# Performance work log

Measured on AMD Instinct MI355X. Metric: run time of the kernel, lower is better.

The kernel has to match this reference:

```python
import jax, jax.numpy as jnp
import numpy as np

B, MAX_S, HID = 128, 4096, 5120
H, D_NOPE, D_ROPE, D_V = 128, 128, 64, 128
KV_SIZE = 512 + 64  # kv_lora_rank + qk_rope_head_dim = 576


def setup_inputs() -> dict:
    key = jax.random.key(0)
    ks = jax.random.split(key, 8)
    seq_lens = jax.random.randint(ks[0], (B,), 1, MAX_S)
    return {
        "hidden_states": jax.random.normal(ks[1], (B, 1, HID), jnp.float32),
        "k_cache": jax.random.normal(ks[2], (B, MAX_S, D_NOPE), jnp.float32),
        "v_cache": jax.random.normal(ks[3], (B, MAX_S, D_V), jnp.float32),
        "Wq": jax.random.normal(ks[4], (HID, H * (D_NOPE + D_ROPE)), jnp.float32) * 0.02,
        "Wkv": jax.random.normal(ks[5], (HID, KV_SIZE), jnp.float32) * 0.02,
        "Wo": jax.random.normal(ks[6], (H * D_V, HID), jnp.float32) * 0.02,
        "positions": seq_lens - 1,
        "slot_mapping": seq_lens - 1,
        "seq_lens": seq_lens,
    }


def reference(hidden_states, k_cache, v_cache, Wq, Wkv, Wo, positions, slot_mapping, seq_lens):
    h = hidden_states[:, -1, :]                        # [B, HID] last-token decode
    q = (h @ Wq).reshape(B, H, D_NOPE + D_ROPE)        # [B, H, 192]
    kv = h @ Wkv                                       # [B, 576]
    q_nope = q[:, :, :D_NOPE]                          # [B, H, 128]
    k_new = kv[:, :D_NOPE]                             # [B, 128]
    v_new = kv[:, D_NOPE:D_NOPE + D_V]                 # [B, 128]

    b_idx = jnp.arange(B)
    kc = k_cache.at[b_idx, slot_mapping].set(k_new)    # write new token into paged cache
    vc = v_cache.at[b_idx, slot_mapping].set(v_new)

    scale = D_NOPE ** -0.5
    scores = jnp.einsum('bhd,bsd->bhs', q_nope, kc) * scale  # MQA: 1 kv head broadcast
    valid = jnp.arange(MAX_S)[None, :] < seq_lens[:, None]   # [B, S]
    scores = jnp.where(valid[:, None, :], scores, jnp.float32(-1e30))
    p = jax.nn.softmax(scores, axis=-1)
    attn = jnp.einsum('bhs,bsd->bhd', p, vc)           # [B, H, 128]

    return attn.reshape(B, 1, H * D_V) @ Wo            # [B, 1, HID]
```

## Files before the change

### kernel.cpp

```cpp
#include <hip/hip_runtime.h>
#include <hip/hip_bf16.h>

typedef __attribute__((ext_vector_type(4))) float f32x4;
typedef __attribute__((ext_vector_type(8))) short bf16x8;
typedef __attribute__((ext_vector_type(2))) unsigned int u32x2;
typedef __attribute__((ext_vector_type(4))) unsigned int u32x4;

static __device__ __forceinline__ unsigned short f2bf(float f) {
    unsigned u = __builtin_bit_cast(unsigned, f);
    u += 0x7fffu + ((u >> 16) & 1u);
    return (unsigned short)(u >> 16);
}
static __device__ __forceinline__ unsigned pack2(float a, float b) {
    __hip_bfloat162 h = __float22bfloat162_rn(make_float2(a, b));
    unsigned u;
    __builtin_memcpy(&u, &h, 4);
    return u;
}

static __device__ __forceinline__ void bar_nodrain() {
    __builtin_amdgcn_sched_barrier(0);
    asm volatile("s_waitcnt lgkmcnt(0)" ::: "memory");
    __builtin_amdgcn_s_barrier();
    __builtin_amdgcn_sched_barrier(0);
}

__global__ __launch_bounds__(256)
void cvt_bf16(const float* __restrict__ in, unsigned* __restrict__ out, int n8)
{
    const int i = blockIdx.x * 256 + threadIdx.x;
    if (i >= n8) return;
    f32x4 a = ((const f32x4*)in)[2 * i];
    f32x4 b = ((const f32x4*)in)[2 * i + 1];
    u32x4 p = { pack2(a[0], a[1]), pack2(a[2], a[3]), pack2(b[0], b[1]), pack2(b[2], b[3]) };
    ((u32x4*)out)[i] = p;
}

template<int COLMAP>
__global__ __launch_bounds__(256, 4)
void gemm128(const unsigned short* __restrict__ Ah, int lda,
             const float* __restrict__ Bm, int ldb,
             float* __restrict__ Cp, int ldc,
             int kchunk, int nsplit)
{
    __shared__ __align__(16) unsigned short As[128 * 72];
    __shared__ __align__(16) unsigned short Bs[64 * 66];

    const int tid = threadIdx.x;
    const int w = tid >> 6, l = tid & 63, lg = l >> 4, l15 = l & 15;
    const int bx = blockIdx.x / nsplit;
    const int by = blockIdx.x % nsplit;
    const int n0 = bx * 64;
    const int pcol = COLMAP ? ((n0 >> 7) * 192 + (n0 & 127)) : n0;
    const size_t k0base = (size_t)by * (size_t)kchunk;
    float* __restrict__ C = Cp + (size_t)by * ((size_t)128 * (size_t)ldc);

    const int ar = tid >> 1;
    const int ac = (tid & 1) * 32;
    const int bnb = (tid & 15) * 4;
    const int bkk = tid >> 4;

    u32x4 aReg[4];
    f32x4 b0Reg[2][2], b1Reg[2][2];

    auto loadA = [&](size_t k0) {
#pragma unroll
        for (int k = 0; k < 4; k++)
            aReg[k] = *(const u32x4*)(Ah + (size_t)ar * lda + k0 + ac + 8 * k);
    };
    auto storeA = [&]() {
#pragma unroll
        for (int k = 0; k < 4; k++)
            *(u32x4*)&As[ar * 72 + ac + 8 * k] = aReg[k];
    };
    auto loadB = [&](f32x4 (&bR)[2][2], size_t k0) {
#pragma unroll
        for (int i = 0; i < 2; i++) {
            const float* bp = Bm + (k0 + (size_t)(2 * (bkk + 16 * i))) * (size_t)ldb + pcol + bnb;
            bR[i][0] = *(const f32x4*)bp;
            bR[i][1] = *(const f32x4*)(bp + ldb);
        }
    };
    auto storeB = [&](f32x4 (&bR)[2][2]) {
        unsigned* bd = (unsigned*)Bs;
#pragma unroll
        for (int i = 0; i < 2; i++)
#pragma unroll
            for (int j = 0; j < 4; j++)
                bd[(bnb + j) * 33 + bkk + 16 * i] = pack2(bR[i][0][j], bR[i][1][j]);
    };

    f32x4 acc[2][4];
    const f32x4 fzero = {0.f, 0.f, 0.f, 0.f};
#pragma unroll
    for (int a = 0; a < 2; a++)
#pragma unroll
        for (int b2 = 0; b2 < 4; b2++) acc[a][b2] = fzero;

    auto mfmaStep = [&]() {
#pragma unroll
        for (int ks = 0; ks < 2; ks++) {
            bf16x8 bfr[4];
#pragma unroll
            for (int nf = 0; nf < 4; nf++)
                bfr[nf] = *(const bf16x8*)&Bs[(16 * nf + l15) * 66 + 32 * ks + 8 * lg];
#pragma unroll
            for (int mf = 0; mf < 2; mf++) {
                bf16x8 af = *(const bf16x8*)&As[(32 * w + 16 * mf + l15) * 72 + 32 * ks + 8 * lg];
#pragma unroll
                for (int nf = 0; nf < 4; nf++)
                    acc[mf][nf] = __builtin_amdgcn_mfma_f32_16x16x32_bf16(af, bfr[nf], acc[mf][nf], 0, 0, 0);
            }
        }
    };

    const int nst = kchunk >> 6;
    auto kof = [&](int t) { return k0base + (size_t)(t << 6); };

    loadA(kof(0));
    loadB(b0Reg, kof(0));
    if (nst > 1) loadB(b1Reg, kof(1));

    for (int t = 0; t < nst; t += 2) {
        storeA(); storeB(b0Reg);
        bar_nodrain();
        if (t + 1 < nst) loadA(kof(t + 1));
        if (t + 2 < nst) loadB(b0Reg, kof(t + 2));
        __builtin_amdgcn_sched_barrier(0);
        mfmaStep();
        bar_nodrain();
        if (t + 1 < nst) {
            storeA(); storeB(b1Reg);
            bar_nodrain();
            if (t + 2 < nst) loadA(kof(t + 2));
            if (t + 3 < nst) loadB(b1Reg, kof(t + 3));
            __builtin_amdgcn_sched_barrier(0);
            mfmaStep();
            bar_nodrain();
        }
    }
#pragma unroll
    for (int mf = 0; mf < 2; mf++) {
#pragma unroll
        for (int nf = 0; nf < 4; nf++) {
            const int m0 = 32 * w + 16 * mf + 4 * lg;
            const int cn = n0 + 16 * nf + l15;
#pragma unroll
            for (int r = 0; r < 4; r++)
                C[(size_t)(m0 + r) * ldc + cn] = acc[mf][nf][r];
        }
    }
}

__global__ __launch_bounds__(256)
void reduce_f32(const float* __restrict__ in, float* __restrict__ out, int n4, int ns)
{
    const int i = blockIdx.x * 256 + threadIdx.x;
    if (i >= n4) return;
    const f32x4* in4 = (const f32x4*)in;
    f32x4 s = in4[i];
    for (int j = 1; j < ns; j++) s += in4[i + (size_t)j * n4];
    ((f32x4*)out)[i] = s;
}

__global__ __launch_bounds__(256)
void reduce_q_bf16(const float* __restrict__ in, unsigned* __restrict__ out)
{
    const int i = blockIdx.x * 256 + threadIdx.x;
    const f32x4* in4 = (const f32x4*)in;
    f32x4 s = in4[i] + in4[i + 524288] + in4[i + 2 * 524288] + in4[i + 3 * 524288];
    const float scale = 0.088388347648318447f;
    s *= scale;
    u32x2 p = { pack2(s[0], s[1]), pack2(s[2], s[3]) };
    *(u32x2*)&out[2 * i] = p;
}

#define NSPLIT 8
#define CHUNK_T 8
#define KVSPLIT 16

__global__ __launch_bounds__(512, 4)
void attn_fwd(const float* __restrict__ kc, const float* __restrict__ vc,
              const unsigned short* __restrict__ qb, const float* __restrict__ kvp,
              const int* __restrict__ seq_lens, const int* __restrict__ slot_map,
              float* __restrict__ Opart, float* __restrict__ m_ws, float* __restrict__ l_ws)
{
    __shared__ __align__(16) unsigned short Ks [64 * 136];
    __shared__ __align__(16) unsigned short Vts[128 * 72];
    __shared__ __align__(16) unsigned short Ps [128 * 72];
    __shared__ float knew_s[128];
    __shared__ float vnew_s[128];

    const int b = blockIdx.x, split = blockIdx.y;
    const int seq = seq_lens[b], slot = slot_map[b];
    const int nt = (seq + 63) >> 6;
    const int t0 = split * CHUNK_T;
    const int t1 = min(t0 + CHUNK_T, nt);
    const int slotTile = slot >> 6;

    const int tid = threadIdx.x, w = tid >> 6, l = tid & 63, lg = l >> 4, l15 = l & 15;
    const int h = 16 * w + l15;

    float m_run = -__builtin_inff(), l_run = 0.0f;

    if (t0 < t1) {
        if (slotTile >= t0 && slotTile < t1 && tid < 256) {
            float s = 0.f;
#pragma unroll
            for (int j = 0; j < KVSPLIT; j++) s += kvp[j * 32768 + b * 256 + tid];
            if (tid < 128) knew_s[tid] = s;
            else           vnew_s[tid - 128] = s;
        }

        bf16x8 qf[4];
        {
            const unsigned short* qrow = qb + (size_t)b * 16384 + (size_t)h * 128;
#pragma unroll
            for (int ks = 0; ks < 4; ks++)
                qf[ks] = *(const bf16x8*)(qrow + 32 * ks + 8 * lg);
        }

        f32x4 kReg[4];
        f32x4 vReg[2][2];
        const int kr  = tid >> 3;
        const int kcb = (tid & 7) * 16;
        const int vsp = tid & 31;
        const int vdq = tid >> 5;

        auto loadKV = [&](int t) {
            const int s0 = t << 6;
            const float* ksrc = kc + ((size_t)b * 4096 + s0 + kr) * 128 + kcb;
#pragma unroll
            for (int c = 0; c < 4; c++) kReg[c] = *(const f32x4*)(ksrc + 4 * c);
#pragma unroll
            for (int i = 0; i < 2; i++) {
                const int d4 = 4 * vdq + 64 * i;
                const float* r1 = vc + ((size_t)b * 4096 + s0 + 2 * vsp) * 128 + d4;
                vReg[i][0] = *(const f32x4*)r1;
                vReg[i][1] = *(const f32x4*)(r1 + 128);
            }
        };
        auto storeKV = [&]() {
            u32x4 w0 = { pack2(kReg[0][0], kReg[0][1]), pack2(kReg[0][2], kReg[0][3]),
                         pack2(kReg[1][0], kReg[1][1]), pack2(kReg[1][2], kReg[1][3]) };
            u32x4 w1 = { pack2(kReg[2][0], kReg[2][1]), pack2(kReg[2][2], kReg[2][3]),
                         pack2(kReg[3][0], kReg[3][1]), pack2(kReg[3][2], kReg[3][3]) };
            *(u32x4*)&Ks[kr * 136 + kcb] = w0;
            *(u32x4*)&Ks[kr * 136 + kcb + 8] = w1;
            unsigned* vt = (unsigned*)Vts;
#pragma unroll
            for (int i = 0; i < 2; i++)
#pragma unroll
                for (int j = 0; j < 4; j++)
                    vt[(4 * vdq + 64 * i + j) * 36 + vsp] = pack2(vReg[i][0][j], vReg[i][1][j]);
        };

        f32x4 accO[8];
        const f32x4 fzero = {0.f, 0.f, 0.f, 0.f};
#pragma unroll
        for (int i = 0; i < 8; i++) accO[i] = fzero;

        loadKV(t0);
        for (int t = t0; t < t1; ++t) {
            const int s0 = t << 6;
            storeKV();
            bar_nodrain();
            if (t == slotTile) {
                if (tid < 128) {
                    const int sloc = slot & 63;
                    Ks [sloc * 136 + tid] = f2bf(knew_s[tid]);
                    Vts[tid * 72 + sloc]  = f2bf(vnew_s[tid]);
                }
                bar_nodrain();
            }
            if (t + 1 < t1) loadKV(t + 1);
            __builtin_amdgcn_sched_barrier(0);

            f32x4 accS[4];
#pragma unroll
            for (int sf = 0; sf < 4; sf++) accS[sf] = fzero;
#pragma unroll
            for (int ks = 0; ks < 4; ks++) {
#pragma unroll
                for (int sf = 0; sf < 4; sf++) {
                    bf16x8 kf = *(const bf16x8*)&Ks[(16 * sf + l15) * 136 + 32 * ks + 8 * lg];
                    accS[sf] = __builtin_amdgcn_mfma_f32_16x16x32_bf16(kf, qf[ks], accS[sf], 0, 0, 0);
                }
            }
            float tmax = -__builtin_inff();
#pragma unroll
            for (int sf = 0; sf < 4; sf++) {
#pragma unroll
                for (int r = 0; r < 4; r++) {
                    const int s = s0 + 16 * sf + 4 * lg + r;
                    float sc = (s < seq) ? accS[sf][r] : -__builtin_inff();
                    accS[sf][r] = sc;
                    tmax = fmaxf(tmax, sc);
                }
            }
            tmax = fmaxf(tmax, __shfl_xor(tmax, 16));
            tmax = fmaxf(tmax, __shfl_xor(tmax, 32));
            const float mnew = fmaxf(m_run, tmax);
            const float so = __expf(m_run - mnew);
            float lsum = 0.f;
#pragma unroll
            for (int sf = 0; sf < 4; sf++) {
#pragma unroll
                for (int r = 0; r < 4; r++) {
                    const float p = __expf(accS[sf][r] - mnew);
                    accS[sf][r] = p;
                    lsum += p;
                }
            }
            lsum += __shfl_xor(lsum, 16);
            lsum += __shfl_xor(lsum, 32);
            l_run = l_run * so + lsum;
            m_run = mnew;
#pragma unroll
            for (int i = 0; i < 8; i++) accO[i] *= so;

            {
                unsigned* pd = (unsigned*)Ps;
#pragma unroll
                for (int sf = 0; sf < 4; sf++) {
                    pd[h * 36 + 8 * sf + 2 * lg + 0] = pack2(accS[sf][0], accS[sf][1]);
                    pd[h * 36 + 8 * sf + 2 * lg + 1] = pack2(accS[sf][2], accS[sf][3]);
                }
            }
            bf16x8 pf[2];
#pragma unroll
            for (int ks = 0; ks < 2; ks++)
                pf[ks] = *(const bf16x8*)&Ps[h * 72 + 32 * ks + 8 * lg];
#pragma unroll
            for (int df = 0; df < 8; df++) {
#pragma unroll
                for (int ks = 0; ks < 2; ks++) {
                    bf16x8 vf = *(const bf16x8*)&Vts[(16 * df + l15) * 72 + 32 * ks + 8 * lg];
                    accO[df] = __builtin_amdgcn_mfma_f32_16x16x32_bf16(vf, pf[ks], accO[df], 0, 0, 0);
                }
            }
            bar_nodrain();
        }
        const size_t base = ((size_t)(b * NSPLIT + split)) * 16384 + (size_t)h * 128;
#pragma unroll
        for (int df = 0; df < 8; df++)
            *(f32x4*)&Opart[base + 16 * df + 4 * lg] = accO[df];
    }
    if (lg == 0) {
        m_ws[(b * NSPLIT + split) * 128 + h] = m_run;
        l_ws[(b * NSPLIT + split) * 128 + h] = l_run;
    }
}

__global__ __launch_bounds__(256)
void combine8(const float* __restrict__ Opart, const float* __restrict__ m_ws,
              const float* __restrict__ l_ws, unsigned* __restrict__ attn_bf)
{
    const int idx = blockIdx.x * 256 + threadIdx.x;
    const int d4 = (idx & 31) * 4;
    const int hh = (idx >> 5) & 127;
    const int b = idx >> 12;

    float m = -__builtin_inff();
    float mv[NSPLIT], lv[NSPLIT];
#pragma unroll
    for (int j = 0; j < NSPLIT; j++) {
        mv[j] = m_ws[(b * NSPLIT + j) * 128 + hh];
        lv[j] = l_ws[(b * NSPLIT + j) * 128 + hh];
        m = fmaxf(m, mv[j]);
    }
    f32x4 o = {0.f, 0.f, 0.f, 0.f};
    float lsum = 0.f;
#pragma unroll
    for (int j = 0; j < NSPLIT; j++) {
        const float a = (lv[j] > 0.f) ? __expf(mv[j] - m) : 0.f;
        lsum += a * lv[j];
        if (a > 0.f) {
            f32x4 oj = *(const f32x4*)&Opart[((size_t)(b * NSPLIT + j)) * 16384 + (size_t)hh * 128 + d4];
            o += oj * a;
        }
    }
    o *= (1.0f / lsum);
    u32x2 p = { pack2(o[0], o[1]), pack2(o[2], o[3]) };
    *(u32x2*)&attn_bf[(size_t)b * 8192 + (size_t)hh * 64 + (d4 >> 1)] = p;
}

extern "C" void kernel_launch(void* const* d_in, const int* in_sizes, int n_in,
                              void* d_out, int out_size, void* d_ws, size_t ws_size,
                              hipStream_t stream)
{
    const float* hidden  = (const float*)d_in[0];
    const float* k_cache = (const float*)d_in[1];
    const float* v_cache = (const float*)d_in[2];
    const float* Wq      = (const float*)d_in[3];
    const float* Wkv     = (const float*)d_in[4];
    const float* Wo      = (const float*)d_in[5];
    const int* slot_map  = (const int*)d_in[7];
    const int* seq_lens  = (const int*)d_in[8];
    float* out = (float*)d_out;

    float* ws      = (float*)d_ws;
    float* hb      = ws;
    float* qp      = ws + 327680;
    float* qb      = ws + 8716288;
    float* kvp     = ws + 9764864;
    float* attn_bf = ws + 10289152;
    float* Opart   = ws + 11337728;
    float* m_ws    = ws + 28114944;
    float* l_ws    = ws + 28246016;
    float* outp    = ws + 28377088;

    cvt_bf16<<<dim3(320), 256, 0, stream>>>(hidden, (unsigned*)hb, 81920);
    gemm128<0><<<dim3(4 * 16), 256, 0, stream>>>((const unsigned short*)hb, 5120, Wkv, 576, kvp, 256, 320, 16);
    gemm128<1><<<dim3(256 * 4), 256, 0, stream>>>((const unsigned short*)hb, 5120, Wq, 24576, qp, 16384, 1280, 4);
    reduce_q_bf16<<<dim3(2048), 256, 0, stream>>>(qp, (unsigned*)qb);
    attn_fwd<<<dim3(128, NSPLIT), 512, 0, stream>>>(k_cache, v_cache, (const unsigned short*)qb,
                                                    kvp, seq_lens, slot_map, Opart, m_ws, l_ws);
    combine8<<<dim3(2048), 256, 0, stream>>>(Opart, m_ws, l_ws, (unsigned*)attn_bf);
    gemm128<0><<<dim3(80 * 16), 256, 0, stream>>>((const unsigned short*)attn_bf, 16384, Wo, 5120, outp, 5120, 1024, 16);
    reduce_f32<<<dim3(640), 256, 0, stream>>>(outp, out, 163840, 16);
}
```

Measured before the change: 322.1 us.

## Store split-K and attention partials in bf16 and fuse Q/KV projection launches

Split-K GEMM partials for the Q projection and output projection, and the per-split attention partial outputs, are now written and read as bf16 instead of fp32. This halves intermediate workspace traffic. The Q and KV projection GEMMs are merged into one launch that dispatches on block index, which removes a launch and lets the small KV GEMM overlap with the Q GEMM. The cost is extra rounding of partial sums before reduction, which loosens accuracy.

```diff
diff --git a/kernel.cpp b/kernel.cpp
--- a/kernel.cpp
+++ b/kernel.cpp
@@ -16,6 +16,12 @@
     unsigned u;
     __builtin_memcpy(&u, &h, 4);
     return u;
+}
+static __device__ __forceinline__ float bf2f(unsigned short s) {
+    unsigned u = (unsigned)s << 16;
+    float f;
+    __builtin_memcpy(&f, &u, 4);
+    return f;
 }
 
 static __device__ __forceinline__ void bar_nodrain() {
@@ -36,24 +42,21 @@
     ((u32x4*)out)[i] = p;
 }
 
-template<int COLMAP>
-__global__ __launch_bounds__(256, 4)
-void gemm128(const unsigned short* __restrict__ Ah, int lda,
-             const float* __restrict__ Bm, int ldb,
-             float* __restrict__ Cp, int ldc,
-             int kchunk, int nsplit)
-{
-    __shared__ __align__(16) unsigned short As[128 * 72];
-    __shared__ __align__(16) unsigned short Bs[64 * 66];
-
+template<int CBF16, int COLMAP>
+__device__ __forceinline__
+void gemm_body(const unsigned short* __restrict__ Ah, int lda,
+               const float* __restrict__ Bm, int ldb,
+               void* __restrict__ Cp, int ldc,
+               int kchunk, int nsplit, int bidx,
+               unsigned short* As, unsigned short* Bs)
+{
     const int tid = threadIdx.x;
     const int w = tid >> 6, l = tid & 63, lg = l >> 4, l15 = l & 15;
-    const int bx = blockIdx.x / nsplit;
-    const int by = blockIdx.x % nsplit;
+    const int bx = bidx / nsplit;
+    const int by = bidx % nsplit;
     const int n0 = bx * 64;
     const int pcol = COLMAP ? ((n0 >> 7) * 192 + (n0 & 127)) : n0;
     const size_t k0base = (size_t)by * (size_t)kchunk;
-    float* __restrict__ C = Cp + (size_t)by * ((size_t)128 * (size_t)ldc);
 
     const int ar = tid >> 1;
     const int ac = (tid & 1) * 32;
@@ -145,34 +148,65 @@
         for (int nf = 0; nf < 4; nf++) {
             const int m0 = 32 * w + 16 * mf + 4 * lg;
             const int cn = n0 + 16 * nf + l15;
-#pragma unroll
-            for (int r = 0; r < 4; r++)
-                C[(size_t)(m0 + r) * ldc + cn] = acc[mf][nf][r];
-        }
-    }
+            if (CBF16) {
+                unsigned short* Ch = (unsigned short*)Cp + (size_t)by * ((size_t)128 * (size_t)ldc);
+#pragma unroll
+                for (int r = 0; r < 4; r++)
+                    Ch[(size_t)(m0 + r) * ldc + cn] = f2bf(acc[mf][nf][r]);
+            } else {
+                float* Cf = (float*)Cp + (size_t)by * ((size_t)128 * (size_t)ldc);
+#pragma unroll
+                for (int r = 0; r < 4; r++)
+                    Cf[(size_t)(m0 + r) * ldc + cn] = acc[mf][nf][r];
+            }
+        }
+    }
+}
+
+#define QBLOCKS 1024
+
+__global__ __launch_bounds__(256, 4)
+void proj_fused(const unsigned short* __restrict__ hb,
+                const float* __restrict__ Wq, const float* __restrict__ Wkv,
+                unsigned short* __restrict__ qp, float* __restrict__ kvp)
+{
+    __shared__ __align__(16) unsigned short As[128 * 72];
+    __shared__ __align__(16) unsigned short Bs[64 * 66];
+    if (blockIdx.x < QBLOCKS)
+        gemm_body<1, 1>(hb, 5120, Wq, 24576, qp, 16384, 1280, 4, blockIdx.x, As, Bs);
+    else
+        gemm_body<0, 0>(hb, 5120, Wkv, 576, kvp, 256, 320, 16, blockIdx.x - QBLOCKS, As, Bs);
+}
+
+__global__ __launch_bounds__(256, 4)
+void gemm_out(const unsigned short* __restrict__ Ah, const float* __restrict__ Wo,
+              unsigned short* __restrict__ outp)
+{
+    __shared__ __align__(16) unsigned short As[128 * 72];
+    __shared__ __align__(16) unsigned short Bs[64 * 66];
+    gemm_body<1, 0>(Ah, 16384, Wo, 5120, outp, 5120, 1024, 16, blockIdx.x, As, Bs);
 }
 
 __global__ __launch_bounds__(256)
-void reduce_f32(const float* __restrict__ in, float* __restrict__ out, int n4, int ns)
+void reduce_q_bf16(const unsigned short* __restrict__ in, unsigned* __restrict__ out)
 {
     const int i = blockIdx.x * 256 + threadIdx.x;
-    if (i >= n4) return;
-    const f32x4* in4 = (const f32x4*)in;
-    f32x4 s = in4[i];
-    for (int j = 1; j < ns; j++) s += in4[i + (size_t)j * n4];
-    ((f32x4*)out)[i] = s;
-}
-
-__global__ __launch_bounds__(256)
-void reduce_q_bf16(const float* __restrict__ in, unsigned* __restrict__ out)
-{
-    const int i = blockIdx.x * 256 + threadIdx.x;
-    const f32x4* in4 = (const f32x4*)in;
-    f32x4 s = in4[i] + in4[i + 524288] + in4[i + 2 * 524288] + in4[i + 3 * 524288];
+    const u32x4* in4 = (const u32x4*)in;
+    u32x4 v0 = in4[i];
+    u32x4 v1 = in4[i + 262144];
+    u32x4 v2 = in4[i + 2 * 262144];
+    u32x4 v3 = in4[i + 3 * 262144];
     const float scale = 0.088388347648318447f;
-    s *= scale;
-    u32x2 p = { pack2(s[0], s[1]), pack2(s[2], s[3]) };
-    *(u32x2*)&out[2 * i] = p;
+    u32x4 r;
+#pragma unroll
+    for (int wd = 0; wd < 4; wd++) {
+        float lo = bf2f((unsigned short)(v0[wd] & 0xffff)) + bf2f((unsigned short)(v1[wd] & 0xffff))
+                 + bf2f((unsigned short)(v2[wd] & 0xffff)) + bf2f((unsigned short)(v3[wd] & 0xffff));
+        float hi = bf2f((unsigned short)(v0[wd] >> 16)) + bf2f((unsigned short)(v1[wd] >> 16))
+                 + bf2f((unsigned short)(v2[wd] >> 16)) + bf2f((unsigned short)(v3[wd] >> 16));
+        r[wd] = pack2(lo * scale, hi * scale);
+    }
+    ((u32x4*)out)[i] = r;
 }
 
 #define NSPLIT 8
@@ -183,7 +217,7 @@
 void attn_fwd(const float* __restrict__ kc, const float* __restrict__ vc,
               const unsigned short* __restrict__ qb, const float* __restrict__ kvp,
               const int* __restrict__ seq_lens, const int* __restrict__ slot_map,
-              float* __restrict__ Opart, float* __restrict__ m_ws, float* __restrict__ l_ws)
+              unsigned short* __restrict__ Opart, float* __restrict__ m_ws, float* __restrict__ l_ws)
 {
     __shared__ __align__(16) unsigned short Ks [64 * 136];
     __shared__ __align__(16) unsigned short Vts[128 * 72];
@@ -341,10 +375,12 @@
             }
             bar_nodrain();
         }
-        const size_t base = ((size_t)(b * NSPLIT + split)) * 16384 + (size_t)h * 128;
-#pragma unroll
-        for (int df = 0; df < 8; df++)
-            *(f32x4*)&Opart[base + 16 * df + 4 * lg] = accO[df];
+        unsigned short* ob = Opart + ((size_t)(b * NSPLIT + split)) * 16384 + (size_t)h * 128;
+#pragma unroll
+        for (int df = 0; df < 8; df++) {
+            u32x2 p = { pack2(accO[df][0], accO[df][1]), pack2(accO[df][2], accO[df][3]) };
+            *(u32x2*)&ob[16 * df + 4 * lg] = p;
+        }
     }
     if (lg == 0) {
         m_ws[(b * NSPLIT + split) * 128 + h] = m_run;
@@ -353,7 +389,7 @@
 }
 
 __global__ __launch_bounds__(256)
-void combine8(const float* __restrict__ Opart, const float* __restrict__ m_ws,
+void combine8(const unsigned short* __restrict__ Opart, const float* __restrict__ m_ws,
               const float* __restrict__ l_ws, unsigned* __restrict__ attn_bf)
 {
     const int idx = blockIdx.x * 256 + threadIdx.x;
@@ -376,13 +412,31 @@
         const float a = (lv[j] > 0.f) ? __expf(mv[j] - m) : 0.f;
         lsum += a * lv[j];
         if (a > 0.f) {
-            f32x4 oj = *(const f32x4*)&Opart[((size_t)(b * NSPLIT + j)) * 16384 + (size_t)hh * 128 + d4];
+            u32x2 v = *(const u32x2*)&Opart[((size_t)(b * NSPLIT + j)) * 16384 + (size_t)hh * 128 + d4];
+            f32x4 oj = { bf2f((unsigned short)(v[0] & 0xffff)), bf2f((unsigned short)(v[0] >> 16)),
+                         bf2f((unsigned short)(v[1] & 0xffff)), bf2f((unsigned short)(v[1] >> 16)) };
             o += oj * a;
         }
     }
     o *= (1.0f / lsum);
     u32x2 p = { pack2(o[0], o[1]), pack2(o[2], o[3]) };
     *(u32x2*)&attn_bf[(size_t)b * 8192 + (size_t)hh * 64 + (d4 >> 1)] = p;
+}
+
+__global__ __launch_bounds__(256)
+void reduce_out_f32(const unsigned short* __restrict__ in, float* __restrict__ out)
+{
+    const int i = blockIdx.x * 256 + threadIdx.x;
+    f32x4 s = {0.f, 0.f, 0.f, 0.f};
+#pragma unroll
+    for (int j = 0; j < 16; j++) {
+        u32x2 v = *(const u32x2*)&in[(size_t)j * 655360 + 4 * (size_t)i];
+        s[0] += bf2f((unsigned short)(v[0] & 0xffff));
+        s[1] += bf2f((unsigned short)(v[0] >> 16));
+        s[2] += bf2f((unsigned short)(v[1] & 0xffff));
+        s[3] += bf2f((unsigned short)(v[1] >> 16));
+    }
+    ((f32x4*)out)[i] = s;
 }
 
 extern "C" void kernel_launch(void* const* d_in, const int* in_sizes, int n_in,
@@ -399,24 +453,23 @@
     const int* seq_lens  = (const int*)d_in[8];
     float* out = (float*)d_out;
 
-    float* ws      = (float*)d_ws;
-    float* hb      = ws;
-    float* qp      = ws + 327680;
-    float* qb      = ws + 8716288;
-    float* kvp     = ws + 9764864;
-    float* attn_bf = ws + 10289152;
-    float* Opart   = ws + 11337728;
-    float* m_ws    = ws + 28114944;
-    float* l_ws    = ws + 28246016;
-    float* outp    = ws + 28377088;
+    float* ws = (float*)d_ws;
+    unsigned short* hb      = (unsigned short*)(ws);
+    unsigned short* qp      = (unsigned short*)(ws + 327680);
+    unsigned short* qb      = (unsigned short*)(ws + 4521984);
+    float*          kvp     = ws + 5570560;
+    unsigned short* attn_bf = (unsigned short*)(ws + 6094848);
+    unsigned short* Opart   = (unsigned short*)(ws + 7143424);
+    float*          m_ws    = ws + 15532032;
+    float*          l_ws    = ws + 15663104;
+    unsigned short* outp    = (unsigned short*)(ws + 15794176);
 
     cvt_bf16<<<dim3(320), 256, 0, stream>>>(hidden, (unsigned*)hb, 81920);
-    gemm128<0><<<dim3(4 * 16), 256, 0, stream>>>((const unsigned short*)hb, 5120, Wkv, 576, kvp, 256, 320, 16);
-    gemm128<1><<<dim3(256 * 4), 256, 0, stream>>>((const unsigned short*)hb, 5120, Wq, 24576, qp, 16384, 1280, 4);
-    reduce_q_bf16<<<dim3(2048), 256, 0, stream>>>(qp, (unsigned*)qb);
-    attn_fwd<<<dim3(128, NSPLIT), 512, 0, stream>>>(k_cache, v_cache, (const unsigned short*)qb,
-                                                    kvp, seq_lens, slot_map, Opart, m_ws, l_ws);
+    proj_fused<<<dim3(QBLOCKS + 64), 256, 0, stream>>>(hb, Wq, Wkv, qp, kvp);
+    reduce_q_bf16<<<dim3(1024), 256, 0, stream>>>(qp, (unsigned*)qb);
+    attn_fwd<<<dim3(128, NSPLIT), 512, 0, stream>>>(k_cache, v_cache, qb, kvp,
+                                                    seq_lens, slot_map, Opart, m_ws, l_ws);
     combine8<<<dim3(2048), 256, 0, stream>>>(Opart, m_ws, l_ws, (unsigned*)attn_bf);
-    gemm128<0><<<dim3(80 * 16), 256, 0, stream>>>((const unsigned short*)attn_bf, 16384, Wo, 5120, outp, 5120, 1024, 16);
-    reduce_f32<<<dim3(640), 256, 0, stream>>>(outp, out, 163840, 16);
-}
+    gemm_out<<<dim3(80 * 16), 256, 0, stream>>>(attn_bf, Wo, outp);
+    reduce_out_f32<<<dim3(640), 256, 0, stream>>>(outp, out);
+}
```

Result: no change. 325.2 us (+1.0%).
